# Kernel optimization log

Hardware: AMD Instinct MI355X
Metric: run time of the kernel (lower is better)

Reference implementation:

```python
import jax, jax.numpy as jnp
import numpy as np

B, R, L, D, F = 64, 50, 15, 1024, 4096  # batch, num_boxes, max_phrase_len, pooling_dim, densecap_feat_dim


def setup_inputs() -> dict:
    key = jax.random.key(0)
    k1, k2, k3, k4 = jax.random.split(key, 4)
    features = jax.random.normal(k1, (B, R, F), dtype=jnp.float32)
    # zero-padded phrase token embeddings per region
    phrase_lengths = jax.random.randint(k2, (B, R), 1, L + 1, dtype=jnp.int32)
    phrases = jax.random.normal(k3, (B, R, L, D), dtype=jnp.float32)
    tok_mask = (jnp.arange(L)[None, None, :] < phrase_lengths[:, :, None]).astype(jnp.float32)
    phrases = phrases * tok_mask[..., None]  # zero padding beyond each phrase length
    # image_pass Linear params (xavier_uniform weight, zero bias)
    limit = float(np.sqrt(6.0 / (F + D)))
    W = jax.random.uniform(k4, (D, F), dtype=jnp.float32, minval=-limit, maxval=limit)
    b = jnp.zeros((D,), dtype=jnp.float32)
    return {"features": features, "phrases": phrases, "W": W, "b": b,
            "phrase_lengths": phrase_lengths}


def reference(features, phrases, W, b, phrase_lengths):
    # segment-mean over phrase tokens: sum of zero-padded tokens / true length
    mean_phrase = jnp.sum(phrases, axis=2) / phrase_lengths[:, :, None].astype(phrases.dtype)  # [B,R,D]
    vis = jax.nn.relu(jnp.einsum('brf,df->brd', features, W) + b)  # [B,R,D]
    return jnp.concatenate([vis, mean_phrase], axis=2)  # [B,R,2D]
```

## Files before the change

### kernel.cpp

```cpp
#include <hip/hip_runtime.h>

#define NB   64
#define NR   50
#define LTOK 15
#define DIM  1024
#define FEAT 4096
#define MTOT (NB*NR)
#define OSTRIDE (2*DIM)

typedef __attribute__((ext_vector_type(8))) short bf16x8;
typedef __attribute__((ext_vector_type(4))) float f32x4;

__global__ __launch_bounds__(256) void mean_pool_kernel(
    const float* __restrict__ phrases,
    const int*   __restrict__ lengths,
    float*       __restrict__ out)
{
    const int br = blockIdx.x;
    const int d4 = threadIdx.x;
    const float4* p = reinterpret_cast<const float4*>(
        phrases + (size_t)br * LTOK * DIM) + d4;

    float4 acc = make_float4(0.f, 0.f, 0.f, 0.f);
    #pragma unroll
    for (int l = 0; l < LTOK; ++l) {
        float4 v = p[(size_t)l * (DIM / 4)];
        acc.x += v.x; acc.y += v.y; acc.z += v.z; acc.w += v.w;
    }
    const float inv = 1.0f / (float)lengths[br];
    acc.x *= inv; acc.y *= inv; acc.z *= inv; acc.w *= inv;

    reinterpret_cast<float4*>(out + (size_t)br * OSTRIDE + DIM)[d4] = acc;
}

#define BM 128
#define BN 128
#define BK 32
#define LDSP 40

__device__ __forceinline__ unsigned short bf16_rne(float f) {
    unsigned int u = __builtin_bit_cast(unsigned int, f);
    unsigned int r = (u + 0x7fffu + ((u >> 16) & 1u)) >> 16;
    return (unsigned short)r;
}
__device__ __forceinline__ float bf16_to_f(unsigned short h) {
    return __builtin_bit_cast(float, (unsigned int)h << 16);
}

__device__ __forceinline__ void split4(const float4 v, ushort4& h, ushort4& l) {
    h.x = bf16_rne(v.x); l.x = bf16_rne(v.x - bf16_to_f(h.x));
    h.y = bf16_rne(v.y); l.y = bf16_rne(v.y - bf16_to_f(h.y));
    h.z = bf16_rne(v.z); l.z = bf16_rne(v.z - bf16_to_f(h.z));
    h.w = bf16_rne(v.w); l.w = bf16_rne(v.w - bf16_to_f(h.w));
}

__global__ __launch_bounds__(256, 1) void gemm_relu_mfma(
    const float* __restrict__ A,
    const float* __restrict__ Bw,
    const float* __restrict__ bias,
    float*       __restrict__ out)
{
    __shared__ __align__(16) unsigned short Ah[BM][LDSP];
    __shared__ __align__(16) unsigned short Al[BM][LDSP];
    __shared__ __align__(16) unsigned short Bh[BN][LDSP];
    __shared__ __align__(16) unsigned short Bl[BN][LDSP];

    const int tid = threadIdx.x;
    const int m0  = blockIdx.y * BM;
    const int n0  = blockIdx.x * BN;

    const int srow = tid >> 3;
    const int scol = (tid & 7) * 4;

    const float* Aptr = A  + (size_t)(m0 + srow) * FEAT + scol;
    const float* Bptr = Bw + (size_t)(n0 + srow) * FEAT + scol;

    const int lane = tid & 63;
    const int wr   = ((tid >> 6) >> 1) * 64;
    const int wc   = ((tid >> 6) & 1) * 64;
    const int fr   = lane & 15;
    const int fk   = (lane >> 4) * 8;

    f32x4 acc[4][4] = {};

    float4 pa[4], pb[4];
    #pragma unroll
    for (int p = 0; p < 4; ++p) {
        pa[p] = *reinterpret_cast<const float4*>(Aptr + (size_t)(p * 32) * FEAT);
        pb[p] = *reinterpret_cast<const float4*>(Bptr + (size_t)(p * 32) * FEAT);
    }

    const int NK = FEAT / BK;
    for (int kt = 0; kt < NK; ++kt) {
        __syncthreads();

        #pragma unroll
        for (int p = 0; p < 4; ++p) {
            const int r = srow + p * 32;
            ushort4 h, l;
            split4(pa[p], h, l);
            *reinterpret_cast<ushort4*>(&Ah[r][scol]) = h;
            *reinterpret_cast<ushort4*>(&Al[r][scol]) = l;
            split4(pb[p], h, l);
            *reinterpret_cast<ushort4*>(&Bh[r][scol]) = h;
            *reinterpret_cast<ushort4*>(&Bl[r][scol]) = l;
        }
        __syncthreads();

        if (kt + 1 < NK) {
            const float* An = Aptr + (size_t)(kt + 1) * BK;
            const float* Bn = Bptr + (size_t)(kt + 1) * BK;
            #pragma unroll
            for (int p = 0; p < 4; ++p) {
                pa[p] = *reinterpret_cast<const float4*>(An + (size_t)(p * 32) * FEAT);
                pb[p] = *reinterpret_cast<const float4*>(Bn + (size_t)(p * 32) * FEAT);
            }
        }

        bf16x8 fah[4], fal[4], fbh[4], fbl[4];
        #pragma unroll
        for (int m = 0; m < 4; ++m) {
            fah[m] = *reinterpret_cast<const bf16x8*>(&Ah[wr + m * 16 + fr][fk]);
            fal[m] = *reinterpret_cast<const bf16x8*>(&Al[wr + m * 16 + fr][fk]);
        }
        #pragma unroll
        for (int n = 0; n < 4; ++n) {
            fbh[n] = *reinterpret_cast<const bf16x8*>(&Bh[wc + n * 16 + fr][fk]);
            fbl[n] = *reinterpret_cast<const bf16x8*>(&Bl[wc + n * 16 + fr][fk]);
        }

        #pragma unroll
        for (int m = 0; m < 4; ++m) {
            #pragma unroll
            for (int n = 0; n < 4; ++n) {
                acc[m][n] = __builtin_amdgcn_mfma_f32_16x16x32_bf16(
                    fah[m], fbl[n], acc[m][n], 0, 0, 0);
                acc[m][n] = __builtin_amdgcn_mfma_f32_16x16x32_bf16(
                    fal[m], fbh[n], acc[m][n], 0, 0, 0);
                acc[m][n] = __builtin_amdgcn_mfma_f32_16x16x32_bf16(
                    fah[m], fbh[n], acc[m][n], 0, 0, 0);
            }
        }
    }

    const int orow0 = m0 + wr + (lane >> 4) * 4;
    const int ocol0 = n0 + wc + fr;
    #pragma unroll
    for (int n = 0; n < 4; ++n) {
        const float bv = bias[ocol0 + n * 16];
        #pragma unroll
        for (int m = 0; m < 4; ++m) {
            #pragma unroll
            for (int r = 0; r < 4; ++r) {
                float v = acc[m][n][r] + bv;
                v = fmaxf(v, 0.f);
                out[(size_t)(orow0 + m * 16 + r) * OSTRIDE + (ocol0 + n * 16)] = v;
            }
        }
    }
}

extern "C" void kernel_launch(void* const* d_in, const int* in_sizes, int n_in,
                              void* d_out, int out_size, void* d_ws, size_t ws_size,
                              hipStream_t stream) {
    const float* features = (const float*)d_in[0];
    const float* phrases  = (const float*)d_in[1];
    const float* W        = (const float*)d_in[2];
    const float* bias     = (const float*)d_in[3];
    const int*   lengths  = (const int*)d_in[4];
    float* out = (float*)d_out;

    mean_pool_kernel<<<dim3(MTOT), dim3(256), 0, stream>>>(phrases, lengths, out);

    gemm_relu_mfma<<<dim3(DIM / BN, MTOT / BM), dim3(256), 0, stream>>>(
        features, W, bias, out);
}
```

Before: 513.1 us.

## Pre-split operands to bf16 hi/lo in workspace and split-K GEMM with async LDS loads

Adds a pre-pass that splits features and W into truncated bf16 hi/lo arrays in workspace. The GEMM then streams these through direct global-to-LDS loads with double buffering and split-K across 4 partitions, each handling a subset of the three hi/lo product passes. Mean pooling is folded into the same launch, and a separate epilogue kernel reduces the partials and applies bias and ReLU. This removes per-tile conversion work and raises occupancy and parallelism, at the cost of extra global traffic for the split arrays and partial buffers, plus two more launches.

Measured after the change: 428.8 us. 1.2x faster.

```diff
diff --git a/kernel.cpp b/kernel.cpp
--- a/kernel.cpp
+++ b/kernel.cpp
@@ -11,16 +11,181 @@
 typedef __attribute__((ext_vector_type(8))) short bf16x8;
 typedef __attribute__((ext_vector_type(4))) float f32x4;
 
+#define WS_AH 0ull
+#define WS_AL 26214400ull
+#define WS_BH 52428800ull
+#define WS_BL 60817408ull
+#define WS_PB 69206016ull
+#define WS_NEED 121634816ull
+
+#define NSPLIT 4
+#define KSTEPS_TOTAL 384
+#define KS_PER_SPLIT 96
+#define GEMM_BLOCKS 800
+
+#define GLOAD16(gsrc, ldst)                                                   \
+    __builtin_amdgcn_global_load_lds(                                         \
+        (__attribute__((address_space(1))) void*)(gsrc),                      \
+        (__attribute__((address_space(3))) void*)(ldst), 16, 0, 0)
+
+__device__ __forceinline__ void split_trunc(float x, unsigned short& h, unsigned short& l) {
+    unsigned int u = __builtin_bit_cast(unsigned int, x);
+    h = (unsigned short)(u >> 16);
+    float r = x - __builtin_bit_cast(float, u & 0xffff0000u);
+    l = (unsigned short)(__builtin_bit_cast(unsigned int, r) >> 16);
+}
+
+__global__ __launch_bounds__(256) void split_kernel(
+    const float* __restrict__ A, const float* __restrict__ W,
+    unsigned short* __restrict__ Ah, unsigned short* __restrict__ Al,
+    unsigned short* __restrict__ Bh, unsigned short* __restrict__ Bl)
+{
+    const int NA4 = MTOT * FEAT / 4;
+    const int NW4 = DIM * FEAT / 4;
+    for (int i = blockIdx.x * 256 + threadIdx.x; i < NA4 + NW4;
+         i += gridDim.x * 256) {
+        const bool isA = i < NA4;
+        const int  j   = isA ? i : i - NA4;
+        const float4 v = isA ? reinterpret_cast<const float4*>(A)[j]
+                             : reinterpret_cast<const float4*>(W)[j];
+        ushort4 h, l;
+        split_trunc(v.x, h.x, l.x); split_trunc(v.y, h.y, l.y);
+        split_trunc(v.z, h.z, l.z); split_trunc(v.w, h.w, l.w);
+        if (isA) {
+            reinterpret_cast<ushort4*>(Ah)[j] = h;
+            reinterpret_cast<ushort4*>(Al)[j] = l;
+        } else {
+            reinterpret_cast<ushort4*>(Bh)[j] = h;
+            reinterpret_cast<ushort4*>(Bl)[j] = l;
+        }
+    }
+}
+
+__global__ __launch_bounds__(256, 3) void gemm_mp_kernel(
+    const unsigned short* __restrict__ Ah, const unsigned short* __restrict__ Al,
+    const unsigned short* __restrict__ Bh, const unsigned short* __restrict__ Bl,
+    const float* __restrict__ phrases, const int* __restrict__ lengths,
+    float* __restrict__ pbuf, float* __restrict__ out)
+{
+    if (blockIdx.x >= GEMM_BLOCKS) {
+        const int br = blockIdx.x - GEMM_BLOCKS;
+        const int d4 = threadIdx.x;
+        const float4* p = reinterpret_cast<const float4*>(
+            phrases + (size_t)br * LTOK * DIM) + d4;
+        float4 acc = make_float4(0.f, 0.f, 0.f, 0.f);
+        #pragma unroll
+        for (int l = 0; l < LTOK; ++l) {
+            float4 v = p[(size_t)l * (DIM / 4)];
+            acc.x += v.x; acc.y += v.y; acc.z += v.z; acc.w += v.w;
+        }
+        const float inv = 1.0f / (float)lengths[br];
+        acc.x *= inv; acc.y *= inv; acc.z *= inv; acc.w *= inv;
+        reinterpret_cast<float4*>(out + (size_t)br * OSTRIDE + DIM)[d4] = acc;
+        return;
+    }
+
+    __shared__ unsigned short At[2][128][32];
+    __shared__ unsigned short Bt[2][128][32];
+
+    const int bid  = blockIdx.x;
+    const int nt   = bid & 7;
+    const int rest = bid >> 3;
+    const int mt   = rest % 25;
+    const int q    = rest / 25;
+
+    const int tid  = threadIdx.x;
+    const int lane = tid & 63;
+    const int w    = tid >> 6;
+    const int wr   = (w >> 1) * 64;
+    const int wc   = (w & 1) * 64;
+    const int fr   = lane & 15;
+    const int fk   = (lane >> 4) * 8;
+
+    const int c0    = w * 2;
+    const int srow  = lane >> 2;
+    const int skoff = (lane & 3) * 8;
+    const unsigned aoff0 = (unsigned)(mt * 128 + 16 * c0      + srow) * FEAT + skoff;
+    const unsigned aoff1 = (unsigned)(mt * 128 + 16 * (c0+1)  + srow) * FEAT + skoff;
+    const unsigned boff0 = (unsigned)(nt * 128 + 16 * c0      + srow) * FEAT + skoff;
+    const unsigned boff1 = (unsigned)(nt * 128 + 16 * (c0+1)  + srow) * FEAT + skoff;
+
+    auto stage = [&](int buf, int s) {
+        const unsigned short* aS = (s < 128) ? Ah : (s < 256 ? Al : Ah);
+        const unsigned short* bS = (s < 256) ? Bh : Bl;
+        const unsigned kk = (unsigned)(s & 127) * 32;
+        GLOAD16(aS + aoff0 + kk, &At[buf][16 * c0][0]);
+        GLOAD16(aS + aoff1 + kk, &At[buf][16 * c0 + 16][0]);
+        GLOAD16(bS + boff0 + kk, &Bt[buf][16 * c0][0]);
+        GLOAD16(bS + boff1 + kk, &Bt[buf][16 * c0 + 16][0]);
+    };
+
+    f32x4 acc[4][4] = {};
+    const int s0 = q * KS_PER_SPLIT;
+
+    stage(0, s0);
+    __syncthreads();
+
+    for (int i = 0; i < KS_PER_SPLIT; ++i) {
+        const int buf = i & 1;
+        if (i + 1 < KS_PER_SPLIT) stage(buf ^ 1, s0 + i + 1);
+
+        bf16x8 a[4], b[4];
+        #pragma unroll
+        for (int m = 0; m < 4; ++m)
+            a[m] = *reinterpret_cast<const bf16x8*>(&At[buf][wr + m * 16 + fr][fk]);
+        #pragma unroll
+        for (int n = 0; n < 4; ++n)
+            b[n] = *reinterpret_cast<const bf16x8*>(&Bt[buf][wc + n * 16 + fr][fk]);
+
+        #pragma unroll
+        for (int m = 0; m < 4; ++m)
+            #pragma unroll
+            for (int n = 0; n < 4; ++n)
+                acc[m][n] = __builtin_amdgcn_mfma_f32_16x16x32_bf16(
+                    a[m], b[n], acc[m][n], 0, 0, 0);
+
+        __syncthreads();
+    }
+
+    const int prow0 = mt * 128 + wr + (lane >> 4) * 4;
+    const int pcol0 = nt * 128 + wc + fr;
+    float* pq = pbuf + (size_t)q * MTOT * DIM;
+    #pragma unroll
+    for (int m = 0; m < 4; ++m)
+        #pragma unroll
+        for (int n = 0; n < 4; ++n)
+            #pragma unroll
+            for (int r = 0; r < 4; ++r)
+                pq[(size_t)(prow0 + m * 16 + r) * DIM + (pcol0 + n * 16)] =
+                    acc[m][n][r];
+}
+
+__global__ __launch_bounds__(256) void epi_kernel(
+    const float* __restrict__ pbuf, const float* __restrict__ bias,
+    float* __restrict__ out)
+{
+    const int r = blockIdx.x;
+    const int j = threadIdx.x;
+    const size_t qs = (size_t)MTOT * (DIM / 4);
+    const float4* p = reinterpret_cast<const float4*>(pbuf) + (size_t)r * (DIM / 4) + j;
+    float4 s0 = p[0], s1 = p[qs], s2 = p[2 * qs], s3 = p[3 * qs];
+    const float4 bv = reinterpret_cast<const float4*>(bias)[j];
+    float4 v;
+    v.x = fmaxf(s0.x + s1.x + s2.x + s3.x + bv.x, 0.f);
+    v.y = fmaxf(s0.y + s1.y + s2.y + s3.y + bv.y, 0.f);
+    v.z = fmaxf(s0.z + s1.z + s2.z + s3.z + bv.z, 0.f);
+    v.w = fmaxf(s0.w + s1.w + s2.w + s3.w + bv.w, 0.f);
+    reinterpret_cast<float4*>(out + (size_t)r * OSTRIDE)[j] = v;
+}
+
 __global__ __launch_bounds__(256) void mean_pool_kernel(
-    const float* __restrict__ phrases,
-    const int*   __restrict__ lengths,
-    float*       __restrict__ out)
+    const float* __restrict__ phrases, const int* __restrict__ lengths,
+    float* __restrict__ out)
 {
     const int br = blockIdx.x;
     const int d4 = threadIdx.x;
     const float4* p = reinterpret_cast<const float4*>(
         phrases + (size_t)br * LTOK * DIM) + d4;
-
     float4 acc = make_float4(0.f, 0.f, 0.f, 0.f);
     #pragma unroll
     for (int l = 0; l < LTOK; ++l) {
@@ -29,7 +194,6 @@
     }
     const float inv = 1.0f / (float)lengths[br];
     acc.x *= inv; acc.y *= inv; acc.z *= inv; acc.w *= inv;
-
     reinterpret_cast<float4*>(out + (size_t)br * OSTRIDE + DIM)[d4] = acc;
 }
 
@@ -46,7 +210,6 @@
 __device__ __forceinline__ float bf16_to_f(unsigned short h) {
     return __builtin_bit_cast(float, (unsigned int)h << 16);
 }
-
 __device__ __forceinline__ void split4(const float4 v, ushort4& h, ushort4& l) {
     h.x = bf16_rne(v.x); l.x = bf16_rne(v.x - bf16_to_f(h.x));
     h.y = bf16_rne(v.y); l.y = bf16_rne(v.y - bf16_to_f(h.y));
@@ -55,26 +218,21 @@
 }
 
 __global__ __launch_bounds__(256, 1) void gemm_relu_mfma(
-    const float* __restrict__ A,
-    const float* __restrict__ Bw,
-    const float* __restrict__ bias,
-    float*       __restrict__ out)
-{
-    __shared__ __align__(16) unsigned short Ah[BM][LDSP];
-    __shared__ __align__(16) unsigned short Al[BM][LDSP];
-    __shared__ __align__(16) unsigned short Bh[BN][LDSP];
-    __shared__ __align__(16) unsigned short Bl[BN][LDSP];
+    const float* __restrict__ A, const float* __restrict__ Bw,
+    const float* __restrict__ bias, float* __restrict__ out)
+{
+    __shared__ __align__(16) unsigned short AhS[BM][LDSP];
+    __shared__ __align__(16) unsigned short AlS[BM][LDSP];
+    __shared__ __align__(16) unsigned short BhS[BN][LDSP];
+    __shared__ __align__(16) unsigned short BlS[BN][LDSP];
 
     const int tid = threadIdx.x;
     const int m0  = blockIdx.y * BM;
     const int n0  = blockIdx.x * BN;
-
     const int srow = tid >> 3;
     const int scol = (tid & 7) * 4;
-
     const float* Aptr = A  + (size_t)(m0 + srow) * FEAT + scol;
     const float* Bptr = Bw + (size_t)(n0 + srow) * FEAT + scol;
-
     const int lane = tid & 63;
     const int wr   = ((tid >> 6) >> 1) * 64;
     const int wc   = ((tid >> 6) & 1) * 64;
@@ -82,31 +240,27 @@
     const int fk   = (lane >> 4) * 8;
 
     f32x4 acc[4][4] = {};
-
     float4 pa[4], pb[4];
     #pragma unroll
     for (int p = 0; p < 4; ++p) {
         pa[p] = *reinterpret_cast<const float4*>(Aptr + (size_t)(p * 32) * FEAT);
         pb[p] = *reinterpret_cast<const float4*>(Bptr + (size_t)(p * 32) * FEAT);
     }
-
     const int NK = FEAT / BK;
     for (int kt = 0; kt < NK; ++kt) {
         __syncthreads();
-
         #pragma unroll
         for (int p = 0; p < 4; ++p) {
             const int r = srow + p * 32;
             ushort4 h, l;
             split4(pa[p], h, l);
-            *reinterpret_cast<ushort4*>(&Ah[r][scol]) = h;
-            *reinterpret_cast<ushort4*>(&Al[r][scol]) = l;
+            *reinterpret_cast<ushort4*>(&AhS[r][scol]) = h;
+            *reinterpret_cast<ushort4*>(&AlS[r][scol]) = l;
             split4(pb[p], h, l);
-            *reinterpret_cast<ushort4*>(&Bh[r][scol]) = h;
-            *reinterpret_cast<ushort4*>(&Bl[r][scol]) = l;
+            *reinterpret_cast<ushort4*>(&BhS[r][scol]) = h;
+            *reinterpret_cast<ushort4*>(&BlS[r][scol]) = l;
         }
         __syncthreads();
-
         if (kt + 1 < NK) {
             const float* An = Aptr + (size_t)(kt + 1) * BK;
             const float* Bn = Bptr + (size_t)(kt + 1) * BK;
@@ -116,47 +270,39 @@
                 pb[p] = *reinterpret_cast<const float4*>(Bn + (size_t)(p * 32) * FEAT);
             }
         }
-
         bf16x8 fah[4], fal[4], fbh[4], fbl[4];
         #pragma unroll
         for (int m = 0; m < 4; ++m) {
-            fah[m] = *reinterpret_cast<const bf16x8*>(&Ah[wr + m * 16 + fr][fk]);
-            fal[m] = *reinterpret_cast<const bf16x8*>(&Al[wr + m * 16 + fr][fk]);
+            fah[m] = *reinterpret_cast<const bf16x8*>(&AhS[wr + m * 16 + fr][fk]);
+            fal[m] = *reinterpret_cast<const bf16x8*>(&AlS[wr + m * 16 + fr][fk]);
         }
         #pragma unroll
         for (int n = 0; n < 4; ++n) {
-            fbh[n] = *reinterpret_cast<const bf16x8*>(&Bh[wc + n * 16 + fr][fk]);
-            fbl[n] = *reinterpret_cast<const bf16x8*>(&Bl[wc + n * 16 + fr][fk]);
-        }
-
-        #pragma unroll
-        for (int m = 0; m < 4; ++m) {
+            fbh[n] = *reinterpret_cast<const bf16x8*>(&BhS[wc + n * 16 + fr][fk]);
+            fbl[n] = *reinterpret_cast<const bf16x8*>(&BlS[wc + n * 16 + fr][fk]);
+        }
+        #pragma unroll
+        for (int m = 0; m < 4; ++m)
             #pragma unroll
             for (int n = 0; n < 4; ++n) {
-                acc[m][n] = __builtin_amdgcn_mfma_f32_16x16x32_bf16(
-                    fah[m], fbl[n], acc[m][n], 0, 0, 0);
-                acc[m][n] = __builtin_amdgcn_mfma_f32_16x16x32_bf16(
-                    fal[m], fbh[n], acc[m][n], 0, 0, 0);
-                acc[m][n] = __builtin_amdgcn_mfma_f32_16x16x32_bf16(
-                    fah[m], fbh[n], acc[m][n], 0, 0, 0);
+                acc[m][n] = __builtin_amdgcn_mfma_f32_16x16x32_bf16(fah[m], fbl[n], acc[m][n], 0, 0, 0);
+                acc[m][n] = __builtin_amdgcn_mfma_f32_16x16x32_bf16(fal[m], fbh[n], acc[m][n], 0, 0, 0);
+                acc[m][n] = __builtin_amdgcn_mfma_f32_16x16x32_bf16(fah[m], fbh[n], acc[m][n], 0, 0, 0);
             }
-        }
-    }
-
+    }
     const int orow0 = m0 + wr + (lane >> 4) * 4;
     const int ocol0 = n0 + wc + fr;
     #pragma unroll
     for (int n = 0; n < 4; ++n) {
         const float bv = bias[ocol0 + n * 16];
         #pragma unroll
-        for (int m = 0; m < 4; ++m) {
+        for (int m = 0; m < 4; ++m)
             #pragma unroll
             for (int r = 0; r < 4; ++r) {
                 float v = acc[m][n][r] + bv;
-                v = fmaxf(v, 0.f);
-                out[(size_t)(orow0 + m * 16 + r) * OSTRIDE + (ocol0 + n * 16)] = v;
+                out[(size_t)(orow0 + m * 16 + r) * OSTRIDE + (ocol0 + n * 16)] =
+                    fmaxf(v, 0.f);
             }
-        }
     }
 }
 
@@ -170,8 +316,22 @@
     const int*   lengths  = (const int*)d_in[4];
     float* out = (float*)d_out;
 
-    mean_pool_kernel<<<dim3(MTOT), dim3(256), 0, stream>>>(phrases, lengths, out);
-
-    gemm_relu_mfma<<<dim3(DIM / BN, MTOT / BM), dim3(256), 0, stream>>>(
-        features, W, bias, out);
-}
+    if (ws_size >= WS_NEED) {
+        char* ws = (char*)d_ws;
+        unsigned short* Ah = (unsigned short*)(ws + WS_AH);
+        unsigned short* Al = (unsigned short*)(ws + WS_AL);
+        unsigned short* Bh = (unsigned short*)(ws + WS_BH);
+        unsigned short* Bl = (unsigned short*)(ws + WS_BL);
+        float* pbuf = (float*)(ws + WS_PB);
+
+        split_kernel<<<dim3(2048), dim3(256), 0, stream>>>(
+            features, W, Ah, Al, Bh, Bl);
+        gemm_mp_kernel<<<dim3(GEMM_BLOCKS + MTOT), dim3(256), 0, stream>>>(
+            Ah, Al, Bh, Bl, phrases, lengths, pbuf, out);
+        epi_kernel<<<dim3(MTOT), dim3(256), 0, stream>>>(pbuf, bias, out);
+    } else {
+        mean_pool_kernel<<<dim3(MTOT), dim3(256), 0, stream>>>(phrases, lengths, out);
+        gemm_relu_mfma<<<dim3(DIM / BN, MTOT / BM), dim3(256), 0, stream>>>(
+            features, W, bias, out);
+    }
+}
```
